# Kernel tuning notes

Measured on AMD Instinct MI355X. Metric: run time of the kernel, lower is better.

## Reference

```python
import jax, jax.numpy as jnp
import numpy as np

B, F, H, E = 16, 128, 144, 24   # batch, frames, num_harmonies, embedding
C0, C1 = 12, 12                 # harmony component dims (root, quality)


def setup_inputs() -> dict:
    key = jax.random.key(0)
    ks = jax.random.split(key, 7)
    note_embedding_seq = jax.random.normal(ks[0], (B, F, E), jnp.float32)
    # one-hot harmony vectors: concat(one_hot(root), one_hot(quality))
    idx = np.arange(H)
    hv = np.zeros((H, E), np.float32)
    hv[idx, idx // C1] = 1.0
    hv[idx, C0 + idx % C1] = 1.0
    harmony_vector = jnp.asarray(np.broadcast_to(hv, (B, H, E)).copy())
    s = 1.0 / np.sqrt(E)
    W0 = jax.random.uniform(ks[1], (C0, C0), jnp.float32, -s, s)
    b0 = jax.random.uniform(ks[2], (C0,), jnp.float32, -s, s)
    W1 = jax.random.uniform(ks[3], (C1, C1), jnp.float32, -s, s)
    b1 = jax.random.uniform(ks[4], (C1,), jnp.float32, -s, s)
    Wc = jax.random.uniform(ks[5], (E, E), jnp.float32, -s, s)
    bc = jax.random.uniform(ks[6], (E,), jnp.float32, -s, s)
    return {"note_embedding_seq": note_embedding_seq, "harmony_vector": harmony_vector,
            "W0": W0, "b0": b0, "W1": W1, "b1": b1, "Wc": Wc, "bc": bc}


def reference(note_embedding_seq, harmony_vector, W0, b0, W1, b1, Wc, bc):
    # HarmonyEncoder: per-component linear then combined linear
    h0 = harmony_vector[..., :C0] @ W0.T + b0
    h1 = harmony_vector[..., C0:] @ W1.T + b1
    q = jnp.concatenate([h0, h1], axis=-1) @ Wc.T + bc          # [B,H,E]

    # Per-segment attention. keys == values, so both the attention logits and
    # the value dot-products reduce to d[b,h,l] = q . k_l.  For segment [s,e]:
    #   score = sum_{l=s..e} softmax_seg(scale*d_l) * d_l
    # which is computed exactly for all segments via cumulative sums.
    scale = 1.0 / jnp.sqrt(jnp.float32(E))
    d = jnp.einsum('bhe,ble->bhl', q, note_embedding_seq)        # [B,H,F]
    m = jnp.max(d * scale, axis=-1, keepdims=True)               # global max: cancels in ratio
    p = jnp.exp(d * scale - m)                                   # [B,H,F]
    num = jnp.cumsum(p * d, axis=-1)                             # [B,H,F]
    den = jnp.cumsum(p, axis=-1)
    num0 = jnp.pad(num, ((0, 0), (0, 0), (1, 0)))[..., :F]       # cumsum up to s-1
    den0 = jnp.pad(den, ((0, 0), (0, 0), (1, 0)))[..., :F]
    dn = num[:, :, None, :] - num0[:, :, :, None]                # [B,H,s,e]
    dd = den[:, :, None, :] - den0[:, :, :, None]
    valid = jnp.triu(jnp.ones((F, F), bool))                     # e >= s
    score = jnp.where(valid, dn / jnp.where(valid, dd, 1.0), 0.0)
    return jnp.transpose(score, (0, 2, 3, 1))                    # [B,F,F,H]
```

## Files before the change

### kernel.cpp

```cpp
#include <hip/hip_runtime.h>
#include <hip/hip_bf16.h>

#define BB 16
#define FF 128
#define HH 144
#define EE 24
#define C0C 12

typedef float v4f __attribute__((ext_vector_type(4)));

#define TABLE_ELEMS (BB * (FF + 1) * HH)

__device__ __forceinline__ float fastdiv(float n, float d) {
    float r = __builtin_amdgcn_rcpf(d);
    r = fmaf(fmaf(-d, r, 1.0f), r, r);
    return n * r;
}

__global__ __launch_bounds__(256) void seg_k1(
    const float* __restrict__ note,
    const float* __restrict__ hv,
    const float* __restrict__ W0,
    const float* __restrict__ b0,
    const float* __restrict__ W1,
    const float* __restrict__ b1,
    const float* __restrict__ Wc,
    const float* __restrict__ bc,
    float* __restrict__ num_t,
    float* __restrict__ den_t)
{
    const int blk = blockIdx.x;
    const int x = blk & 7;
    const int t = blk >> 3;
    const int b = 2 * x + (t >= 9);
    const int tile = (t >= 9) ? t - 9 : t;
    const int h0 = tile * 16;
    const int tid = threadIdx.x;

    __shared__ float s_note[FF * EE];
    __shared__ float s_hcat[16][EE];
    __shared__ float s_q[16][EE];
    __shared__ float s_p[FF][16];
    __shared__ float s_pd[FF][16];
    __shared__ float s_pm[16][16];
    __shared__ float s_m[16];

    const float* nb_ = note + (size_t)b * FF * EE;
    for (int k = tid; k < FF * EE / 4; k += 256)
        reinterpret_cast<v4f*>(s_note)[k] = reinterpret_cast<const v4f*>(nb_)[k];

    for (int idx = tid; idx < 16 * EE; idx += 256) {
        const int hl = idx / EE, e = idx - hl * EE;
        const float* hvb = hv + ((size_t)b * HH + h0 + hl) * EE;
        float acc;
        if (e < C0C) {
            acc = b0[e];
            #pragma unroll
            for (int j = 0; j < C0C; ++j) acc += W0[e * C0C + j] * hvb[j];
        } else {
            const int e1 = e - C0C;
            acc = b1[e1];
            #pragma unroll
            for (int j = 0; j < C0C; ++j) acc += W1[e1 * C0C + j] * hvb[C0C + j];
        }
        s_hcat[hl][e] = acc;
    }
    __syncthreads();
    for (int idx = tid; idx < 16 * EE; idx += 256) {
        const int hl = idx / EE, e = idx - hl * EE;
        float acc = bc[e];
        #pragma unroll
        for (int j = 0; j < EE; ++j) acc += Wc[e * EE + j] * s_hcat[hl][j];
        s_q[hl][e] = acc;
    }
    __syncthreads();

    const int hl = tid & 15;
    const int f0 = tid >> 4;
    const float scale = 0.20412414523193150818f;

    float dv[8];
    float pmax = -3.4e38f;
    #pragma unroll
    for (int k = 0; k < 8; ++k) {
        const int f = f0 + (k << 4);
        float acc = 0.f;
        #pragma unroll
        for (int e = 0; e < EE; ++e) acc += s_q[hl][e] * s_note[f * EE + e];
        dv[k] = acc;
        pmax = fmaxf(pmax, acc);
    }
    s_pm[f0][hl] = pmax * scale;
    __syncthreads();
    if (tid < 16) {
        float m = s_pm[0][tid];
        #pragma unroll
        for (int r = 1; r < 16; ++r) m = fmaxf(m, s_pm[r][tid]);
        s_m[tid] = m;
    }
    __syncthreads();
    const float m = s_m[hl];

    #pragma unroll
    for (int k = 0; k < 8; ++k) {
        const int f = f0 + (k << 4);
        const float p = __expf(dv[k] * scale - m);
        s_p[f][hl] = p;
        s_pd[f][hl] = p * dv[k];
    }
    __syncthreads();

    for (int off = 1; off < FF; off <<= 1) {
        float tp[8], tpd[8];
        #pragma unroll
        for (int k = 0; k < 8; ++k) {
            const int f = f0 + (k << 4);
            tp[k] = (f >= off) ? s_p[f - off][hl] : 0.f;
            tpd[k] = (f >= off) ? s_pd[f - off][hl] : 0.f;
        }
        __syncthreads();
        #pragma unroll
        for (int k = 0; k < 8; ++k) {
            const int f = f0 + (k << 4);
            if (f >= off) { s_p[f][hl] += tp[k]; s_pd[f][hl] += tpd[k]; }
        }
        __syncthreads();
    }

    const size_t base = (size_t)b * (FF + 1) * HH + h0;
    for (int idx4 = tid; idx4 < 512; idx4 += 256) {
        const int f = idx4 >> 2;
        const int hh = (idx4 & 3) * 4;
        *reinterpret_cast<v4f*>(num_t + base + (size_t)(f + 1) * HH + hh) =
            *reinterpret_cast<const v4f*>(&s_pd[f][hh]);
        *reinterpret_cast<v4f*>(den_t + base + (size_t)(f + 1) * HH + hh) =
            *reinterpret_cast<const v4f*>(&s_p[f][hh]);
    }
    if (tid < 16) {
        num_t[base + tid] = 0.f;
        den_t[base + tid] = 0.f;
    }
}

__device__ __forceinline__ void k2_row_half(
    const float* __restrict__ nb, const float* __restrict__ db,
    float* __restrict__ out_b, int s, int tid, int half)
{
    float* ob = out_b + (size_t)s * (FF * HH);

    const int nzr = (s - half + 1) >> 1;
    for (int c = tid; c < nzr * 36; c += 256) {
        const int row2 = c / 36;
        const int col = c - row2 * 36;
        const int row = 2 * row2 + half;
        *reinterpret_cast<v4f*>(ob + (size_t)row * HH + col * 4) = (v4f)(0.f);
    }

    if (tid < 252) {
        const int r = tid / 36;
        const int hq = tid - r * 36;
        const int h = hq * 4;

        const v4f n0 = *reinterpret_cast<const v4f*>(nb + (size_t)s * HH + h);
        const v4f d0 = *reinterpret_cast<const v4f*>(db + (size_t)s * HH + h);

        const int e0 = s + r + 7 * half;
        const float* pn = nb + (size_t)(e0 + 1) * HH + h;
        const float* pd_ = db + (size_t)(e0 + 1) * HH + h;
        float* po = ob + (size_t)e0 * HH + h;

        #pragma unroll 2
        for (int e = e0; e < FF; e += 14) {
            const v4f n1 = *reinterpret_cast<const v4f*>(pn);
            const v4f d1 = *reinterpret_cast<const v4f*>(pd_);
            v4f val;
            val.x = fastdiv(n1.x - n0.x, d1.x - d0.x);
            val.y = fastdiv(n1.y - n0.y, d1.y - d0.y);
            val.z = fastdiv(n1.z - n0.z, d1.z - d0.z);
            val.w = fastdiv(n1.w - n0.w, d1.w - d0.w);
            *reinterpret_cast<v4f*>(po) = val;
            pn += 14 * HH;
            pd_ += 14 * HH;
            po += 14 * HH;
        }
    }
}

__global__ __launch_bounds__(256) void seg_k2(
    const float* __restrict__ num_t,
    const float* __restrict__ den_t,
    float* __restrict__ out)
{
    const int blk = blockIdx.x;
    const int x = blk & 7;
    const int t = blk >> 3;
    const int b = 2 * x + (t >= 128);
    const int j = t & 127;
    const int sp = j >> 1;
    const int half = j & 1;
    const int tid = threadIdx.x;

    const float* nb = num_t + (size_t)b * (FF + 1) * HH;
    const float* db = den_t + (size_t)b * (FF + 1) * HH;
    float* out_b = out + (size_t)b * (FF * FF * HH);

    k2_row_half(nb, db, out_b, sp, tid, half);
    k2_row_half(nb, db, out_b, 127 - sp, tid, half);
}

extern "C" void kernel_launch(void* const* d_in, const int* in_sizes, int n_in,
                              void* d_out, int out_size, void* d_ws, size_t ws_size,
                              hipStream_t stream) {
    const float* note = (const float*)d_in[0];
    const float* hv   = (const float*)d_in[1];
    const float* W0   = (const float*)d_in[2];
    const float* b0   = (const float*)d_in[3];
    const float* W1   = (const float*)d_in[4];
    const float* b1   = (const float*)d_in[5];
    const float* Wc   = (const float*)d_in[6];
    const float* bc   = (const float*)d_in[7];
    float* out = (float*)d_out;

    float* num_t = (float*)d_ws;
    float* den_t = num_t + TABLE_ELEMS;

    seg_k1<<<144, 256, 0, stream>>>(note, hv, W0, b0, W1, b1, Wc, bc, num_t, den_t);
    seg_k2<<<BB * FF, 256, 0, stream>>>(num_t, den_t, out);
}
```

Baseline: 36.58 us.

## Fuse prefix-sum and segment-division kernels into one kernel with recomputation

Merges the two kernels into a single launch of 2304 blocks. Each block recomputes q, the dot products, the softmax weights and the prefix sums for its 16 harmonies in shared memory, then writes 8 output rows from them. This removes the second launch and the global workspace round trip for the num/den tables. The cost is that the small prefix computation is repeated 16 times per batch/harmony tile. Output stores now use 16-float segments per row rather than full 144-float rows, which may coalesce less well.

```diff
diff --git a/kernel.cpp b/kernel.cpp
--- a/kernel.cpp
+++ b/kernel.cpp
@@ -9,15 +9,13 @@
 
 typedef float v4f __attribute__((ext_vector_type(4)));
 
-#define TABLE_ELEMS (BB * (FF + 1) * HH)
-
 __device__ __forceinline__ float fastdiv(float n, float d) {
     float r = __builtin_amdgcn_rcpf(d);
     r = fmaf(fmaf(-d, r, 1.0f), r, r);
     return n * r;
 }
 
-__global__ __launch_bounds__(256) void seg_k1(
+__global__ __launch_bounds__(256) void seg_fused(
     const float* __restrict__ note,
     const float* __restrict__ hv,
     const float* __restrict__ W0,
@@ -26,28 +24,24 @@
     const float* __restrict__ b1,
     const float* __restrict__ Wc,
     const float* __restrict__ bc,
-    float* __restrict__ num_t,
-    float* __restrict__ den_t)
+    float* __restrict__ out)
 {
     const int blk = blockIdx.x;
     const int x = blk & 7;
-    const int t = blk >> 3;
-    const int b = 2 * x + (t >= 9);
-    const int tile = (t >= 9) ? t - 9 : t;
-    const int h0 = tile * 16;
+    const int v = blk >> 3;
+    const int b = 2 * x + (v >= 144);
+    const int w = (v >= 144) ? v - 144 : v;
+    const int hs = w >> 4;
+    const int sg = w & 15;
+    const int h0 = hs * 16;
     const int tid = threadIdx.x;
 
-    __shared__ float s_note[FF * EE];
     __shared__ float s_hcat[16][EE];
     __shared__ float s_q[16][EE];
-    __shared__ float s_p[FF][16];
-    __shared__ float s_pd[FF][16];
+    __shared__ float s_num[FF + 1][16];
+    __shared__ float s_den[FF + 1][16];
     __shared__ float s_pm[16][16];
     __shared__ float s_m[16];
-
-    const float* nb_ = note + (size_t)b * FF * EE;
-    for (int k = tid; k < FF * EE / 4; k += 256)
-        reinterpret_cast<v4f*>(s_note)[k] = reinterpret_cast<const v4f*>(nb_)[k];
 
     for (int idx = tid; idx < 16 * EE; idx += 256) {
         const int hl = idx / EE, e = idx - hl * EE;
@@ -73,20 +67,30 @@
         for (int j = 0; j < EE; ++j) acc += Wc[e * EE + j] * s_hcat[hl][j];
         s_q[hl][e] = acc;
     }
+    if (tid < 16) {
+        s_num[0][tid] = 0.f;
+        s_den[0][tid] = 0.f;
+    }
     __syncthreads();
 
     const int hl = tid & 15;
     const int f0 = tid >> 4;
     const float scale = 0.20412414523193150818f;
+    const float* nb_ = note + (size_t)b * FF * EE;
 
     float dv[8];
     float pmax = -3.4e38f;
     #pragma unroll
     for (int k = 0; k < 8; ++k) {
         const int f = f0 + (k << 4);
+        const float* nr = nb_ + f * EE;
         float acc = 0.f;
         #pragma unroll
-        for (int e = 0; e < EE; ++e) acc += s_q[hl][e] * s_note[f * EE + e];
+        for (int e = 0; e < EE; e += 4) {
+            const v4f nv = *reinterpret_cast<const v4f*>(nr + e);
+            acc += s_q[hl][e] * nv.x + s_q[hl][e + 1] * nv.y
+                 + s_q[hl][e + 2] * nv.z + s_q[hl][e + 3] * nv.w;
+        }
         dv[k] = acc;
         pmax = fmaxf(pmax, acc);
     }
@@ -105,8 +109,8 @@
     for (int k = 0; k < 8; ++k) {
         const int f = f0 + (k << 4);
         const float p = __expf(dv[k] * scale - m);
-        s_p[f][hl] = p;
-        s_pd[f][hl] = p * dv[k];
+        s_num[f + 1][hl] = p * dv[k];
+        s_den[f + 1][hl] = p;
     }
     __syncthreads();
 
@@ -115,97 +119,47 @@
         #pragma unroll
         for (int k = 0; k < 8; ++k) {
             const int f = f0 + (k << 4);
-            tp[k] = (f >= off) ? s_p[f - off][hl] : 0.f;
-            tpd[k] = (f >= off) ? s_pd[f - off][hl] : 0.f;
+            tp[k] = (f >= off) ? s_num[f + 1 - off][hl] : 0.f;
+            tpd[k] = (f >= off) ? s_den[f + 1 - off][hl] : 0.f;
         }
         __syncthreads();
         #pragma unroll
         for (int k = 0; k < 8; ++k) {
             const int f = f0 + (k << 4);
-            if (f >= off) { s_p[f][hl] += tp[k]; s_pd[f][hl] += tpd[k]; }
+            if (f >= off) { s_num[f + 1][hl] += tp[k]; s_den[f + 1][hl] += tpd[k]; }
         }
         __syncthreads();
     }
 
-    const size_t base = (size_t)b * (FF + 1) * HH + h0;
-    for (int idx4 = tid; idx4 < 512; idx4 += 256) {
-        const int f = idx4 >> 2;
-        const int hh = (idx4 & 3) * 4;
-        *reinterpret_cast<v4f*>(num_t + base + (size_t)(f + 1) * HH + hh) =
-            *reinterpret_cast<const v4f*>(&s_pd[f][hh]);
-        *reinterpret_cast<v4f*>(den_t + base + (size_t)(f + 1) * HH + hh) =
-            *reinterpret_cast<const v4f*>(&s_p[f][hh]);
-    }
-    if (tid < 16) {
-        num_t[base + tid] = 0.f;
-        den_t[base + tid] = 0.f;
-    }
-}
+    const int q4 = (tid & 3) * 4;
+    const int er = tid >> 2;
+    float* out_b = out + (size_t)b * (FF * FF * HH) + h0;
 
-__device__ __forceinline__ void k2_row_half(
-    const float* __restrict__ nb, const float* __restrict__ db,
-    float* __restrict__ out_b, int s, int tid, int half)
-{
-    float* ob = out_b + (size_t)s * (FF * HH);
-
-    const int nzr = (s - half + 1) >> 1;
-    for (int c = tid; c < nzr * 36; c += 256) {
-        const int row2 = c / 36;
-        const int col = c - row2 * 36;
-        const int row = 2 * row2 + half;
-        *reinterpret_cast<v4f*>(ob + (size_t)row * HH + col * 4) = (v4f)(0.f);
-    }
-
-    if (tid < 252) {
-        const int r = tid / 36;
-        const int hq = tid - r * 36;
-        const int h = hq * 4;
-
-        const v4f n0 = *reinterpret_cast<const v4f*>(nb + (size_t)s * HH + h);
-        const v4f d0 = *reinterpret_cast<const v4f*>(db + (size_t)s * HH + h);
-
-        const int e0 = s + r + 7 * half;
-        const float* pn = nb + (size_t)(e0 + 1) * HH + h;
-        const float* pd_ = db + (size_t)(e0 + 1) * HH + h;
-        float* po = ob + (size_t)e0 * HH + h;
-
-        #pragma unroll 2
-        for (int e = e0; e < FF; e += 14) {
-            const v4f n1 = *reinterpret_cast<const v4f*>(pn);
-            const v4f d1 = *reinterpret_cast<const v4f*>(pd_);
-            v4f val;
-            val.x = fastdiv(n1.x - n0.x, d1.x - d0.x);
-            val.y = fastdiv(n1.y - n0.y, d1.y - d0.y);
-            val.z = fastdiv(n1.z - n0.z, d1.z - d0.z);
-            val.w = fastdiv(n1.w - n0.w, d1.w - d0.w);
-            *reinterpret_cast<v4f*>(po) = val;
-            pn += 14 * HH;
-            pd_ += 14 * HH;
-            po += 14 * HH;
+    #pragma unroll
+    for (int pp = 0; pp < 4; ++pp) {
+        const int s_lo = sg * 4 + pp;
+        #pragma unroll
+        for (int side = 0; side < 2; ++side) {
+            const int s = side ? 127 - s_lo : s_lo;
+            float* ob = out_b + (size_t)s * (FF * HH);
+            const v4f n0 = *reinterpret_cast<const v4f*>(&s_num[s][q4]);
+            const v4f d0 = *reinterpret_cast<const v4f*>(&s_den[s][q4]);
+            int e = er;
+            #pragma unroll
+            for (int k = 0; k < 2; ++k, e += 64) {
+                v4f val = (v4f)(0.f);
+                if (e >= s) {
+                    const v4f n1 = *reinterpret_cast<const v4f*>(&s_num[e + 1][q4]);
+                    const v4f d1 = *reinterpret_cast<const v4f*>(&s_den[e + 1][q4]);
+                    val.x = fastdiv(n1.x - n0.x, d1.x - d0.x);
+                    val.y = fastdiv(n1.y - n0.y, d1.y - d0.y);
+                    val.z = fastdiv(n1.z - n0.z, d1.z - d0.z);
+                    val.w = fastdiv(n1.w - n0.w, d1.w - d0.w);
+                }
+                *reinterpret_cast<v4f*>(ob + (size_t)e * HH + q4) = val;
+            }
         }
     }
-}
-
-__global__ __launch_bounds__(256) void seg_k2(
-    const float* __restrict__ num_t,
-    const float* __restrict__ den_t,
-    float* __restrict__ out)
-{
-    const int blk = blockIdx.x;
-    const int x = blk & 7;
-    const int t = blk >> 3;
-    const int b = 2 * x + (t >= 128);
-    const int j = t & 127;
-    const int sp = j >> 1;
-    const int half = j & 1;
-    const int tid = threadIdx.x;
-
-    const float* nb = num_t + (size_t)b * (FF + 1) * HH;
-    const float* db = den_t + (size_t)b * (FF + 1) * HH;
-    float* out_b = out + (size_t)b * (FF * FF * HH);
-
-    k2_row_half(nb, db, out_b, sp, tid, half);
-    k2_row_half(nb, db, out_b, 127 - sp, tid, half);
 }
 
 extern "C" void kernel_launch(void* const* d_in, const int* in_sizes, int n_in,
@@ -221,9 +175,5 @@
     const float* bc   = (const float*)d_in[7];
     float* out = (float*)d_out;
 
-    float* num_t = (float*)d_ws;
-    float* den_t = num_t + TABLE_ELEMS;
-
-    seg_k1<<<144, 256, 0, stream>>>(note, hv, W0, b0, W1, b1, Wc, bc, num_t, den_t);
-    seg_k2<<<BB * FF, 256, 0, stream>>>(num_t, den_t, out);
+    seg_fused<<<2304, 256, 0, stream>>>(note, hv, W0, b0, W1, b1, Wc, bc, out);
 }
```

Measured after the change: 44.98 us. 1.23x slower.
